# Optimization experiments

Measured on AMD Instinct MI355X. Metric: run time of the kernel, lower is better.

Reference implementation:

```python
import jax, jax.numpy as jnp
import numpy as np

USER_NUM = 100000
ITEM_NUM = 50000
EMBED = 64
N_LAYERS = 3
E_RATE = 2000000
E_TRUST = 500000
E_PRED = 100000


def setup_inputs() -> dict:
    key = jax.random.key(0)
    ks = jax.random.split(key, 10)
    return {
        "emb_user": jax.random.normal(ks[0], (USER_NUM, EMBED), dtype=jnp.float32),
        "emb_item": jax.random.normal(ks[1], (ITEM_NUM, EMBED), dtype=jnp.float32),
        "rate_u": jax.random.randint(ks[2], (E_RATE,), 0, USER_NUM, dtype=jnp.int32),
        "rate_i": jax.random.randint(ks[3], (E_RATE,), 0, ITEM_NUM, dtype=jnp.int32),
        "trust_src": jax.random.randint(ks[4], (E_TRUST,), 0, USER_NUM, dtype=jnp.int32),
        "trust_dst": jax.random.randint(ks[5], (E_TRUST,), 0, USER_NUM, dtype=jnp.int32),
        "pos_u": jax.random.randint(ks[6], (E_PRED,), 0, USER_NUM, dtype=jnp.int32),
        "pos_i": jax.random.randint(ks[7], (E_PRED,), 0, ITEM_NUM, dtype=jnp.int32),
        "neg_u": jax.random.randint(ks[8], (E_PRED,), 0, USER_NUM, dtype=jnp.int32),
        "neg_i": jax.random.randint(ks[9], (E_PRED,), 0, ITEM_NUM, dtype=jnp.int32),
    }


def _degrees(idx, n):
    # float degree counts, clamped to >=1 (DGL GraphConv clamps zero degrees)
    d = jax.ops.segment_sum(jnp.ones_like(idx, dtype=jnp.float32), idx, num_segments=n)
    return jnp.maximum(d, 1.0)


def _gcn_conv(h_src, src, dst, n_dst, deg_src, deg_dst):
    # GraphConv(norm='both', weight=False, bias=False):
    # out[v] = deg(v)^-1/2 * sum_{u->v} deg(u)^-1/2 * h[u]
    ns = jax.lax.rsqrt(deg_src)
    nd = jax.lax.rsqrt(deg_dst)
    msg = (h_src * ns[:, None])[src]          # [E, D] gather
    agg = jax.ops.segment_sum(msg, dst, num_segments=n_dst)
    return agg * nd[:, None]


def reference(emb_user, emb_item, rate_u, rate_i, trust_src, trust_dst,
              pos_u, pos_i, neg_u, neg_i):
    nU, nI = emb_user.shape[0], emb_item.shape[0]
    deg_u = _degrees(rate_u, nU)       # user degree in rate graph (out for rate, in for rated-by)
    deg_i = _degrees(rate_i, nI)       # item degree in rate graph
    deg_ts = _degrees(trust_src, nU)
    deg_td = _degrees(trust_dst, nU)

    res_u, res_i = emb_user, emb_item
    cur_u, cur_i = emb_user, emb_item
    for _ in range(N_LAYERS):
        # item -> user ('rated-by'): src deg = deg_i, dst deg = deg_u
        new_u = _gcn_conv(cur_i, rate_i, rate_u, nU, deg_i, deg_u)
        # user -> item ('rate')
        new_i = _gcn_conv(cur_u, rate_u, rate_i, nI, deg_u, deg_i)
        # user -> user ('trust'), added into user output
        new_u = new_u + _gcn_conv(cur_u, trust_src, trust_dst, nU, deg_ts, deg_td)
        res_u = res_u + new_u
        res_i = res_i + new_i
        cur_u, cur_i = new_u, new_i

    scale = 1.0 / (N_LAYERS + 1)
    res_u = res_u * scale
    res_i = res_i * scale

    # HeteroDotProductPredictor on 'rate' etype: u_dot_v -> [E, 1]
    pos_score = jnp.sum(res_u[pos_u] * res_i[pos_i], axis=-1, keepdims=True)
    neg_score = jnp.sum(res_u[neg_u] * res_i[neg_i], axis=-1, keepdims=True)
    return pos_score, neg_score
```

## Files before the change

kernel.cpp:

```cpp
#include <hip/hip_runtime.h>
#include <hip/hip_fp16.h>

#define NU 100000
#define NI 50000
#define D  64
#define CAPU 64
#define CAPI 96
#define CAPT 32
#define BS 256

#define NB1 256
#define KPB1 391
#define CAPB1 9216
#define NB2 256
#define KPB2 196
#define CAPB2 9216
#define NB3 128
#define KPB3 782
#define CAPB3 4864
#define NB4 128
#define CAPB4 4864
#define GR 224
#define GT 32

typedef unsigned long long u64;

__global__ void __launch_bounds__(1024) k_binAll(
    const int* __restrict__ ru, const int* __restrict__ ri,
    const int* __restrict__ ts, const int* __restrict__ td,
    int* __restrict__ bc1, int* __restrict__ bc2,
    int* __restrict__ bc3, int* __restrict__ bc4,
    u64* __restrict__ bins1, u64* __restrict__ bins2,
    u64* __restrict__ bins3, u64* __restrict__ bins4,
    int E_rate, int E_trust)
{
    __shared__ int cnt[512];
    __shared__ int base[512];
    int b = blockIdx.x, tid = threadIdx.x;
    if (b < GR) {
        if (tid < 512) cnt[tid] = 0;
        __syncthreads();
        for (int c0 = b * 1024; c0 < E_rate; c0 += GR * 1024) {
            int e = c0 + tid;
            if (e < E_rate) {
                int u = ru[e], it = ri[e];
                atomicAdd(&cnt[u / KPB1], 1);
                atomicAdd(&cnt[256 + it / KPB2], 1);
            }
        }
        __syncthreads();
        if (tid < 256)      base[tid] = atomicAdd(&bc1[tid], cnt[tid]);
        else if (tid < 512) base[tid] = atomicAdd(&bc2[tid - 256], cnt[tid]);
        __syncthreads();
        if (tid < 512) cnt[tid] = 0;
        __syncthreads();
        for (int c0 = b * 1024; c0 < E_rate; c0 += GR * 1024) {
            int e = c0 + tid;
            if (e < E_rate) {
                int u = ru[e], it = ri[e];
                int b1 = u / KPB1, b2 = it / KPB2;
                int r1 = atomicAdd(&cnt[b1], 1);
                int o1 = base[b1] + r1;
                if (o1 < CAPB1) bins1[(size_t)b1 * CAPB1 + o1] = ((u64)u << 32) | (unsigned)it;
                int r2 = atomicAdd(&cnt[256 + b2], 1);
                int o2 = base[256 + b2] + r2;
                if (o2 < CAPB2) bins2[(size_t)b2 * CAPB2 + o2] = ((u64)it << 32) | (unsigned)u;
            }
        }
    } else {
        int bb = b - GR;
        if (tid < 256) cnt[tid] = 0;
        __syncthreads();
        for (int c0 = bb * 1024; c0 < E_trust; c0 += GT * 1024) {
            int e = c0 + tid;
            if (e < E_trust) {
                int s = ts[e], dd = td[e];
                atomicAdd(&cnt[dd / KPB3], 1);
                atomicAdd(&cnt[128 + s / KPB3], 1);
            }
        }
        __syncthreads();
        if (tid < 128)      base[tid] = atomicAdd(&bc3[tid], cnt[tid]);
        else if (tid < 256) base[tid] = atomicAdd(&bc4[tid - 128], cnt[tid]);
        __syncthreads();
        if (tid < 256) cnt[tid] = 0;
        __syncthreads();
        for (int c0 = bb * 1024; c0 < E_trust; c0 += GT * 1024) {
            int e = c0 + tid;
            if (e < E_trust) {
                int s = ts[e], dd = td[e];
                int b3 = dd / KPB3, b4 = s / KPB3;
                int r3 = atomicAdd(&cnt[b3], 1);
                int o3 = base[b3] + r3;
                if (o3 < CAPB3) bins3[(size_t)b3 * CAPB3 + o3] = ((u64)dd << 32) | (unsigned)s;
                int r4 = atomicAdd(&cnt[128 + b4], 1);
                int o4 = base[128 + b4] + r4;
                if (o4 < CAPB4) bins4[(size_t)b4 * CAPB4 + o4] = ((u64)s << 32);
            }
        }
    }
}

__global__ void __launch_bounds__(512) k_buildAll(
    const u64* __restrict__ bins1, const u64* __restrict__ bins2,
    const u64* __restrict__ bins3, const u64* __restrict__ bins4,
    const int* __restrict__ bc1, const int* __restrict__ bc2,
    const int* __restrict__ bc3, const int* __restrict__ bc4,
    int* __restrict__ colU, int* __restrict__ colI, int* __restrict__ colT,
    int* __restrict__ degU, int* __restrict__ degI,
    int* __restrict__ degT, int* __restrict__ degS)
{
    __shared__ int cnt[KPB3];
    int b = blockIdx.x, tid = threadIdx.x;
    const u64* bins; int n, k0, kpb, colcap, nmax; int* col; int* deg;
    if (b < NB1) {
        bins = bins1 + (size_t)b * CAPB1; n = bc1[b]; if (n > CAPB1) n = CAPB1;
        k0 = b * KPB1; kpb = KPB1; colcap = CAPU; col = colU; deg = degU; nmax = NU;
    } else if (b < NB1 + NB2) {
        int q = b - NB1;
        bins = bins2 + (size_t)q * CAPB2; n = bc2[q]; if (n > CAPB2) n = CAPB2;
        k0 = q * KPB2; kpb = KPB2; colcap = CAPI; col = colI; deg = degI; nmax = NI;
    } else if (b < NB1 + NB2 + NB3) {
        int q = b - NB1 - NB2;
        bins = bins3 + (size_t)q * CAPB3; n = bc3[q]; if (n > CAPB3) n = CAPB3;
        k0 = q * KPB3; kpb = KPB3; colcap = CAPT; col = colT; deg = degT; nmax = NU;
    } else {
        int q = b - NB1 - NB2 - NB3;
        bins = bins4 + (size_t)q * CAPB4; n = bc4[q]; if (n > CAPB4) n = CAPB4;
        k0 = q * KPB3; kpb = KPB3; colcap = 0; col = nullptr; deg = degS; nmax = NU;
    }
    for (int t = tid; t < kpb; t += 512) cnt[t] = 0;
    __syncthreads();
    if (col) {
        for (int i = tid; i < n; i += 512) {
            u64 e = bins[i];
            int k = (int)(e >> 32);
            int v = (int)(e & 0xffffffffu);
            int c = atomicAdd(&cnt[k - k0], 1);
            if (c < colcap) col[(size_t)k * colcap + c] = v;
        }
    } else {
        for (int i = tid; i < n; i += 512) {
            int k = (int)(bins[i] >> 32);
            atomicAdd(&cnt[k - k0], 1);
        }
    }
    __syncthreads();
    for (int t = tid; t < kpb; t += 512) {
        int k = k0 + t;
        if (k < nmax) {
            int c = cnt[t];
            if (colcap && c > colcap) c = colcap;
            deg[k] = c;
        }
    }
}

__global__ void k_degrs(const int* __restrict__ degU, const int* __restrict__ degI,
                        const int* __restrict__ degT, const int* __restrict__ degS,
                        float* __restrict__ rs_u, float* __restrict__ rs_i,
                        float* __restrict__ rs_td, float* __restrict__ rs_tsu) {
    int i = blockIdx.x * blockDim.x + threadIdx.x;
    if (i < NU) {
        int a = degU[i]; float ru = rsqrtf((float)(a < 1 ? 1 : a));
        rs_u[i] = ru;
        int b = degT[i]; rs_td[i] = rsqrtf((float)(b < 1 ? 1 : b));
        int c = degS[i]; rs_tsu[i] = rsqrtf((float)(c < 1 ? 1 : c)) / ru;
    }
    if (i < NI) {
        int a = degI[i]; rs_i[i] = rsqrtf((float)(a < 1 ? 1 : a));
    }
}

__device__ __forceinline__ uint2 pack4(float a, float b, float c, float d) {
    __half2 lo = __floats2half2_rn(a, b);
    __half2 hi = __floats2half2_rn(c, d);
    uint2 r;
    r.x = *(unsigned*)&lo;
    r.y = *(unsigned*)&hi;
    return r;
}

__global__ void k_inith(const float* __restrict__ src, const float* __restrict__ rs,
                        uint2* __restrict__ curS, uint2* __restrict__ res, int n16) {
    int i = blockIdx.x * blockDim.x + threadIdx.x;
    if (i >= n16) return;
    float4 v = ((const float4*)src)[i];
    float s = rs[i >> 4];
    res[i]  = pack4(v.x, v.y, v.z, v.w);
    curS[i] = pack4(s * v.x, s * v.y, s * v.z, s * v.w);
}

__global__ void k_zrow(uint2* uA, uint2* uB, uint2* iA, uint2* iB) {
    int t = threadIdx.x;
    int e = t & 15;
    uint2 z; z.x = 0; z.y = 0;
    if (t < 16)      uA[(size_t)NU * 16 + e] = z;
    else if (t < 32) uB[(size_t)NU * 16 + e] = z;
    else if (t < 48) iA[(size_t)NI * 16 + e] = z;
    else             iB[(size_t)NI * 16 + e] = z;
}

__global__ void k_layer(const int* __restrict__ colU, const int* __restrict__ degU,
                        const int* __restrict__ colT, const int* __restrict__ degT,
                        const int* __restrict__ colI, const int* __restrict__ degI,
                        const float* __restrict__ rs_u, const float* __restrict__ rs_i,
                        const float* __restrict__ rs_td, const float* __restrict__ rs_tsu,
                        const uint2* __restrict__ cuR, const uint2* __restrict__ ciS,
                        uint2* __restrict__ nuR, uint2* __restrict__ niS,
                        uint2* __restrict__ resu, uint2* __restrict__ resi) {
    int b = blockIdx.x;
    int m = b % 3;
    int base = b / 3;
    int wid = threadIdx.x >> 6;
    int lane = threadIdx.x & 63;
    int grp = lane >> 4;
    int gl  = lane & 15;
    if (m < 2) {
        int node = ((base * 2 + m) * 4 + wid) * 4 + grp;
        if (node >= NU) return;
        float4 acc = {0.f, 0.f, 0.f, 0.f};
        {
            int bb = node * CAPU, e = bb + degU[node];
            for (int k0 = bb; k0 < e; k0 += 16) {
                int idx = k0 + gl;
                int n = idx < e ? colU[idx] : NI;
                #pragma unroll
                for (int j = 0; j < 16; ++j) {
                    int nn = __shfl(n, j, 16);
                    uint2 q = ciS[(size_t)nn * 16 + gl];
                    float2 f = __half22float2(*(__half2*)&q.x);
                    float2 g = __half22float2(*(__half2*)&q.y);
                    acc.x += f.x; acc.y += f.y; acc.z += g.x; acc.w += g.y;
                }
            }
        }
        float4 acc2 = {0.f, 0.f, 0.f, 0.f};
        {
            int bb = node * CAPT, e = bb + degT[node];
            int sub = gl & 7;
            for (int k0 = bb; k0 < e; k0 += 8) {
                int idx = k0 + sub;
                int n = idx < e ? colT[idx] : NU;
                float w = idx < e ? rs_tsu[n] : 0.f;
                #pragma unroll
                for (int j = 0; j < 8; ++j) {
                    int nn  = __shfl(n, j, 16);
                    float ww = __shfl(w, j, 16);
                    uint2 q = cuR[(size_t)nn * 16 + gl];
                    float2 f = __half22float2(*(__half2*)&q.x);
                    float2 g = __half22float2(*(__half2*)&q.y);
                    acc2.x += ww * f.x; acc2.y += ww * f.y;
                    acc2.z += ww * g.x; acc2.w += ww * g.y;
                }
            }
        }
        float su = rs_u[node], st = rs_td[node];
        float vx = su * acc.x + st * acc2.x;
        float vy = su * acc.y + st * acc2.y;
        float vz = su * acc.z + st * acc2.z;
        float vw = su * acc.w + st * acc2.w;
        size_t o = (size_t)node * 16 + gl;
        nuR[o] = pack4(su * vx, su * vy, su * vz, su * vw);
        uint2 r = resu[o];
        float2 ra = __half22float2(*(__half2*)&r.x);
        float2 rb = __half22float2(*(__half2*)&r.y);
        resu[o] = pack4(ra.x + vx, ra.y + vy, rb.x + vz, rb.y + vw);
    } else {
        int node = (base * 4 + wid) * 4 + grp;
        if (node >= NI) return;
        float4 acc = {0.f, 0.f, 0.f, 0.f};
        {
            int bb = node * CAPI, e = bb + degI[node];
            for (int k0 = bb; k0 < e; k0 += 16) {
                int idx = k0 + gl;
                int n = idx < e ? colI[idx] : NU;
                #pragma unroll
                for (int j = 0; j < 16; ++j) {
                    int nn = __shfl(n, j, 16);
                    uint2 q = cuR[(size_t)nn * 16 + gl];
                    float2 f = __half22float2(*(__half2*)&q.x);
                    float2 g = __half22float2(*(__half2*)&q.y);
                    acc.x += f.x; acc.y += f.y; acc.z += g.x; acc.w += g.y;
                }
            }
        }
        float si = rs_i[node];
        float vx = si * acc.x, vy = si * acc.y, vz = si * acc.z, vw = si * acc.w;
        size_t o = (size_t)node * 16 + gl;
        niS[o] = pack4(si * vx, si * vy, si * vz, si * vw);
        uint2 r = resi[o];
        float2 ra = __half22float2(*(__half2*)&r.x);
        float2 rb = __half22float2(*(__half2*)&r.y);
        resi[o] = pack4(ra.x + vx, ra.y + vy, rb.x + vz, rb.y + vw);
    }
}

__global__ void k_pred(const int* __restrict__ pu, const int* __restrict__ pi,
                       const int* __restrict__ nuv, const int* __restrict__ niv,
                       const __half2* __restrict__ ru, const __half2* __restrict__ ri,
                       float* __restrict__ out, int E) {
    long long tid = (long long)blockIdx.x * blockDim.x + threadIdx.x;
    int e = (int)(tid >> 4);
    int c2 = ((int)tid & 15) * 2;
    if (e >= 2 * E) return;
    int ee = (e < E) ? e : e - E;
    int u  = (e < E) ? pu[ee] : nuv[ee];
    int it = (e < E) ? pi[ee] : niv[ee];
    float2 a0 = __half22float2(ru[(size_t)u  * 32 + c2]);
    float2 a1 = __half22float2(ru[(size_t)u  * 32 + c2 + 1]);
    float2 b0 = __half22float2(ri[(size_t)it * 32 + c2]);
    float2 b1 = __half22float2(ri[(size_t)it * 32 + c2 + 1]);
    float s = a0.x * b0.x + a0.y * b0.y + a1.x * b1.x + a1.y * b1.y;
    s += __shfl_xor(s, 1); s += __shfl_xor(s, 2);
    s += __shfl_xor(s, 4); s += __shfl_xor(s, 8);
    if (((int)tid & 15) == 0) out[e] = s * (1.0f / 16.0f);
}

extern "C" void kernel_launch(void* const* d_in, const int* in_sizes, int n_in,
                              void* d_out, int out_size, void* d_ws, size_t ws_size,
                              hipStream_t stream) {
    const float* emb_u  = (const float*)d_in[0];
    const float* emb_i  = (const float*)d_in[1];
    const int* rate_u   = (const int*)d_in[2];
    const int* rate_i   = (const int*)d_in[3];
    const int* trust_s  = (const int*)d_in[4];
    const int* trust_d  = (const int*)d_in[5];
    const int* pos_u    = (const int*)d_in[6];
    const int* pos_i    = (const int*)d_in[7];
    const int* neg_u    = (const int*)d_in[8];
    const int* neg_i    = (const int*)d_in[9];
    const int E_rate  = in_sizes[2];
    const int E_trust = in_sizes[4];
    const int E_pred  = in_sizes[6];

    int* iw   = (int*)d_ws;
    int* degU = iw;
    int* degI = degU + NU;
    int* degT = degI + NI;
    int* degS = degT + NU;
    int* bc1  = degS + NU;
    int* bc2  = bc1 + NB1;
    int* bc3  = bc2 + NB2;
    int* bc4  = bc3 + NB3;
    int* colU = bc4 + NB4;
    int* colI = colU + (size_t)NU * CAPU;
    int* colT = colI + (size_t)NI * CAPI;
    float* rs_u   = (float*)(colT + (size_t)NU * CAPT);
    float* rs_i   = rs_u  + NU;
    float* rs_td  = rs_i  + NI;
    float* rs_tsu = rs_td + NU;
    uint2* uRA  = (uint2*)(rs_tsu + NU);
    uint2* uRB  = uRA + (size_t)(NU + 1) * 16;
    uint2* iSA  = uRB + (size_t)(NU + 1) * 16;
    uint2* iSB  = iSA + (size_t)(NI + 1) * 16;
    uint2* res_u = iSB + (size_t)(NI + 1) * 16;
    uint2* res_i = res_u + (size_t)NU * 16;
    u64* bins1 = (u64*)uRA;
    u64* bins2 = bins1 + (size_t)NB1 * CAPB1;
    u64* bins3 = bins2 + (size_t)NB2 * CAPB2;
    u64* bins4 = bins3 + (size_t)NB3 * CAPB3;

    hipMemsetAsync(bc1, 0, (NB1 + NB2 + NB3 + NB4) * sizeof(int), stream);

    k_binAll<<<GR + GT, 1024, 0, stream>>>(rate_u, rate_i, trust_s, trust_d,
                                           bc1, bc2, bc3, bc4,
                                           bins1, bins2, bins3, bins4,
                                           E_rate, E_trust);
    k_buildAll<<<NB1 + NB2 + NB3 + NB4, 512, 0, stream>>>(
        bins1, bins2, bins3, bins4, bc1, bc2, bc3, bc4,
        colU, colI, colT, degU, degI, degT, degS);

    k_degrs<<<(NU + BS - 1) / BS, BS, 0, stream>>>(degU, degI, degT, degS,
                                                   rs_u, rs_i, rs_td, rs_tsu);

    k_inith<<<(NU * 16 + BS - 1) / BS, BS, 0, stream>>>(emb_u, rs_u, uRA, res_u, NU * 16);
    k_inith<<<(NI * 16 + BS - 1) / BS, BS, 0, stream>>>(emb_i, rs_i, iSA, res_i, NI * 16);
    k_zrow<<<1, 64, 0, stream>>>(uRA, uRB, iSA, iSB);

    uint2* cu = uRA; uint2* nu_ = uRB;
    uint2* ci = iSA; uint2* ni_ = iSB;
    for (int l = 0; l < 3; ++l) {
        k_layer<<<9375, BS, 0, stream>>>(colU, degU, colT, degT, colI, degI,
                                         rs_u, rs_i, rs_td, rs_tsu,
                                         cu, ci, nu_, ni_, res_u, res_i);
        uint2* t;
        t = cu; cu = nu_; nu_ = t;
        t = ci; ci = ni_; ni_ = t;
    }

    long long tp = (long long)2 * E_pred * 16;
    k_pred<<<(unsigned)((tp + BS - 1) / BS), BS, 0, stream>>>(
        pos_u, pos_i, neg_u, neg_i, (const __half2*)res_u, (const __half2*)res_i,
        (float*)d_out, E_pred);
}
```

Baseline: 366.3 us.

## Pack bins into 32-bit keys, shrink user adjacency to u16, accumulate in half2

Bin entries are packed into 32-bit words holding a local key offset plus the neighbour index, halving bin traffic. The user adjacency list of item ids is stored as 16-bit values, halving those index loads. The layer kernel accumulates rating-neighbour sums in half2 instead of float, and the binning grid is enlarged fourfold. The half-precision accumulation over up to 64-96 neighbours risks precision loss and overflow.

```diff
diff --git a/kernel.cpp b/kernel.cpp
--- a/kernel.cpp
+++ b/kernel.cpp
@@ -3,7 +3,6 @@
 
 #define NU 100000
 #define NI 50000
-#define D  64
 #define CAPU 64
 #define CAPI 96
 #define CAPT 32
@@ -20,18 +19,19 @@
 #define CAPB3 4864
 #define NB4 128
 #define CAPB4 4864
-#define GR 224
-#define GT 32
-
-typedef unsigned long long u64;
+#define GR 896
+#define GT 128
+
+typedef unsigned int u32;
+typedef unsigned short u16;
 
 __global__ void __launch_bounds__(1024) k_binAll(
     const int* __restrict__ ru, const int* __restrict__ ri,
     const int* __restrict__ ts, const int* __restrict__ td,
     int* __restrict__ bc1, int* __restrict__ bc2,
     int* __restrict__ bc3, int* __restrict__ bc4,
-    u64* __restrict__ bins1, u64* __restrict__ bins2,
-    u64* __restrict__ bins3, u64* __restrict__ bins4,
+    u32* __restrict__ bins1, u32* __restrict__ bins2,
+    u32* __restrict__ bins3, u32* __restrict__ bins4,
     int E_rate, int E_trust)
 {
     __shared__ int cnt[512];
@@ -61,10 +61,12 @@
                 int b1 = u / KPB1, b2 = it / KPB2;
                 int r1 = atomicAdd(&cnt[b1], 1);
                 int o1 = base[b1] + r1;
-                if (o1 < CAPB1) bins1[(size_t)b1 * CAPB1 + o1] = ((u64)u << 32) | (unsigned)it;
+                if (o1 < CAPB1)
+                    bins1[(size_t)b1 * CAPB1 + o1] = ((u32)(u - b1 * KPB1) << 16) | (u32)it;
                 int r2 = atomicAdd(&cnt[256 + b2], 1);
                 int o2 = base[256 + b2] + r2;
-                if (o2 < CAPB2) bins2[(size_t)b2 * CAPB2 + o2] = ((u64)it << 32) | (unsigned)u;
+                if (o2 < CAPB2)
+                    bins2[(size_t)b2 * CAPB2 + o2] = ((u32)(it - b2 * KPB2) << 17) | (u32)u;
             }
         }
     } else {
@@ -92,66 +94,93 @@
                 int b3 = dd / KPB3, b4 = s / KPB3;
                 int r3 = atomicAdd(&cnt[b3], 1);
                 int o3 = base[b3] + r3;
-                if (o3 < CAPB3) bins3[(size_t)b3 * CAPB3 + o3] = ((u64)dd << 32) | (unsigned)s;
+                if (o3 < CAPB3)
+                    bins3[(size_t)b3 * CAPB3 + o3] = ((u32)(dd - b3 * KPB3) << 17) | (u32)s;
                 int r4 = atomicAdd(&cnt[128 + b4], 1);
                 int o4 = base[128 + b4] + r4;
-                if (o4 < CAPB4) bins4[(size_t)b4 * CAPB4 + o4] = ((u64)s << 32);
+                if (o4 < CAPB4)
+                    bins4[(size_t)b4 * CAPB4 + o4] = (u32)(s - b4 * KPB3);
             }
         }
     }
 }
 
 __global__ void __launch_bounds__(512) k_buildAll(
-    const u64* __restrict__ bins1, const u64* __restrict__ bins2,
-    const u64* __restrict__ bins3, const u64* __restrict__ bins4,
+    const u32* __restrict__ bins1, const u32* __restrict__ bins2,
+    const u32* __restrict__ bins3, const u32* __restrict__ bins4,
     const int* __restrict__ bc1, const int* __restrict__ bc2,
     const int* __restrict__ bc3, const int* __restrict__ bc4,
-    int* __restrict__ colU, int* __restrict__ colI, int* __restrict__ colT,
+    u16* __restrict__ colU, int* __restrict__ colI, int* __restrict__ colT,
     int* __restrict__ degU, int* __restrict__ degI,
     int* __restrict__ degT, int* __restrict__ degS)
 {
     __shared__ int cnt[KPB3];
     int b = blockIdx.x, tid = threadIdx.x;
-    const u64* bins; int n, k0, kpb, colcap, nmax; int* col; int* deg;
     if (b < NB1) {
-        bins = bins1 + (size_t)b * CAPB1; n = bc1[b]; if (n > CAPB1) n = CAPB1;
-        k0 = b * KPB1; kpb = KPB1; colcap = CAPU; col = colU; deg = degU; nmax = NU;
+        const u32* bins = bins1 + (size_t)b * CAPB1;
+        int n = bc1[b]; if (n > CAPB1) n = CAPB1;
+        int k0 = b * KPB1;
+        for (int t = tid; t < KPB1; t += 512) cnt[t] = 0;
+        __syncthreads();
+        for (int i = tid; i < n; i += 512) {
+            u32 e = bins[i];
+            int ko = e >> 16, v = e & 0xFFFF;
+            int c = atomicAdd(&cnt[ko], 1);
+            if (c < CAPU) colU[(size_t)(k0 + ko) * CAPU + c] = (u16)v;
+        }
+        __syncthreads();
+        for (int t = tid; t < KPB1; t += 512) {
+            int k = k0 + t;
+            if (k < NU) { int c = cnt[t]; if (c > CAPU) c = CAPU; degU[k] = c; }
+        }
     } else if (b < NB1 + NB2) {
         int q = b - NB1;
-        bins = bins2 + (size_t)q * CAPB2; n = bc2[q]; if (n > CAPB2) n = CAPB2;
-        k0 = q * KPB2; kpb = KPB2; colcap = CAPI; col = colI; deg = degI; nmax = NI;
+        const u32* bins = bins2 + (size_t)q * CAPB2;
+        int n = bc2[q]; if (n > CAPB2) n = CAPB2;
+        int k0 = q * KPB2;
+        for (int t = tid; t < KPB2; t += 512) cnt[t] = 0;
+        __syncthreads();
+        for (int i = tid; i < n; i += 512) {
+            u32 e = bins[i];
+            int ko = e >> 17, v = e & 0x1FFFF;
+            int c = atomicAdd(&cnt[ko], 1);
+            if (c < CAPI) colI[(size_t)(k0 + ko) * CAPI + c] = v;
+        }
+        __syncthreads();
+        for (int t = tid; t < KPB2; t += 512) {
+            int k = k0 + t;
+            if (k < NI) { int c = cnt[t]; if (c > CAPI) c = CAPI; degI[k] = c; }
+        }
     } else if (b < NB1 + NB2 + NB3) {
         int q = b - NB1 - NB2;
-        bins = bins3 + (size_t)q * CAPB3; n = bc3[q]; if (n > CAPB3) n = CAPB3;
-        k0 = q * KPB3; kpb = KPB3; colcap = CAPT; col = colT; deg = degT; nmax = NU;
+        const u32* bins = bins3 + (size_t)q * CAPB3;
+        int n = bc3[q]; if (n > CAPB3) n = CAPB3;
+        int k0 = q * KPB3;
+        for (int t = tid; t < KPB3; t += 512) cnt[t] = 0;
+        __syncthreads();
+        for (int i = tid; i < n; i += 512) {
+            u32 e = bins[i];
+            int ko = e >> 17, v = e & 0x1FFFF;
+            int c = atomicAdd(&cnt[ko], 1);
+            if (c < CAPT) colT[(size_t)(k0 + ko) * CAPT + c] = v;
+        }
+        __syncthreads();
+        for (int t = tid; t < KPB3; t += 512) {
+            int k = k0 + t;
+            if (k < NU) { int c = cnt[t]; if (c > CAPT) c = CAPT; degT[k] = c; }
+        }
     } else {
         int q = b - NB1 - NB2 - NB3;
-        bins = bins4 + (size_t)q * CAPB4; n = bc4[q]; if (n > CAPB4) n = CAPB4;
-        k0 = q * KPB3; kpb = KPB3; colcap = 0; col = nullptr; deg = degS; nmax = NU;
-    }
-    for (int t = tid; t < kpb; t += 512) cnt[t] = 0;
-    __syncthreads();
-    if (col) {
-        for (int i = tid; i < n; i += 512) {
-            u64 e = bins[i];
-            int k = (int)(e >> 32);
-            int v = (int)(e & 0xffffffffu);
-            int c = atomicAdd(&cnt[k - k0], 1);
-            if (c < colcap) col[(size_t)k * colcap + c] = v;
-        }
-    } else {
-        for (int i = tid; i < n; i += 512) {
-            int k = (int)(bins[i] >> 32);
-            atomicAdd(&cnt[k - k0], 1);
-        }
-    }
-    __syncthreads();
-    for (int t = tid; t < kpb; t += 512) {
-        int k = k0 + t;
-        if (k < nmax) {
-            int c = cnt[t];
-            if (colcap && c > colcap) c = colcap;
-            deg[k] = c;
+        const u32* bins = bins4 + (size_t)q * CAPB4;
+        int n = bc4[q]; if (n > CAPB4) n = CAPB4;
+        int k0 = q * KPB3;
+        for (int t = tid; t < KPB3; t += 512) cnt[t] = 0;
+        __syncthreads();
+        for (int i = tid; i < n; i += 512) atomicAdd(&cnt[bins[i]], 1);
+        __syncthreads();
+        for (int t = tid; t < KPB3; t += 512) {
+            int k = k0 + t;
+            if (k < NU) degS[k] = cnt[t];
         }
     }
 }
@@ -201,7 +230,7 @@
     else             iB[(size_t)NI * 16 + e] = z;
 }
 
-__global__ void k_layer(const int* __restrict__ colU, const int* __restrict__ degU,
+__global__ void k_layer(const u16* __restrict__ colU, const int* __restrict__ degU,
                         const int* __restrict__ colT, const int* __restrict__ degT,
                         const int* __restrict__ colI, const int* __restrict__ degI,
                         const float* __restrict__ rs_u, const float* __restrict__ rs_i,
@@ -216,25 +245,26 @@
     int lane = threadIdx.x & 63;
     int grp = lane >> 4;
     int gl  = lane & 15;
+    __half2 zero = __floats2half2_rn(0.f, 0.f);
     if (m < 2) {
         int node = ((base * 2 + m) * 4 + wid) * 4 + grp;
         if (node >= NU) return;
-        float4 acc = {0.f, 0.f, 0.f, 0.f};
+        __half2 ha = zero, hb = zero;
         {
             int bb = node * CAPU, e = bb + degU[node];
             for (int k0 = bb; k0 < e; k0 += 16) {
                 int idx = k0 + gl;
-                int n = idx < e ? colU[idx] : NI;
+                int n = idx < e ? (int)colU[idx] : NI;
                 #pragma unroll
                 for (int j = 0; j < 16; ++j) {
                     int nn = __shfl(n, j, 16);
                     uint2 q = ciS[(size_t)nn * 16 + gl];
-                    float2 f = __half22float2(*(__half2*)&q.x);
-                    float2 g = __half22float2(*(__half2*)&q.y);
-                    acc.x += f.x; acc.y += f.y; acc.z += g.x; acc.w += g.y;
+                    ha = __hadd2(ha, *(__half2*)&q.x);
+                    hb = __hadd2(hb, *(__half2*)&q.y);
                 }
             }
         }
+        float2 fa = __half22float2(ha), fb = __half22float2(hb);
         float4 acc2 = {0.f, 0.f, 0.f, 0.f};
         {
             int bb = node * CAPT, e = bb + degT[node];
@@ -256,10 +286,10 @@
             }
         }
         float su = rs_u[node], st = rs_td[node];
-        float vx = su * acc.x + st * acc2.x;
-        float vy = su * acc.y + st * acc2.y;
-        float vz = su * acc.z + st * acc2.z;
-        float vw = su * acc.w + st * acc2.w;
+        float vx = su * fa.x + st * acc2.x;
+        float vy = su * fa.y + st * acc2.y;
+        float vz = su * fb.x + st * acc2.z;
+        float vw = su * fb.y + st * acc2.w;
         size_t o = (size_t)node * 16 + gl;
         nuR[o] = pack4(su * vx, su * vy, su * vz, su * vw);
         uint2 r = resu[o];
@@ -269,7 +299,7 @@
     } else {
         int node = (base * 4 + wid) * 4 + grp;
         if (node >= NI) return;
-        float4 acc = {0.f, 0.f, 0.f, 0.f};
+        __half2 ha = zero, hb = zero;
         {
             int bb = node * CAPI, e = bb + degI[node];
             for (int k0 = bb; k0 < e; k0 += 16) {
@@ -279,14 +309,14 @@
                 for (int j = 0; j < 16; ++j) {
                     int nn = __shfl(n, j, 16);
                     uint2 q = cuR[(size_t)nn * 16 + gl];
-                    float2 f = __half22float2(*(__half2*)&q.x);
-                    float2 g = __half22float2(*(__half2*)&q.y);
-                    acc.x += f.x; acc.y += f.y; acc.z += g.x; acc.w += g.y;
+                    ha = __hadd2(ha, *(__half2*)&q.x);
+                    hb = __hadd2(hb, *(__half2*)&q.y);
                 }
             }
         }
+        float2 fa = __half22float2(ha), fb = __half22float2(hb);
         float si = rs_i[node];
-        float vx = si * acc.x, vy = si * acc.y, vz = si * acc.z, vw = si * acc.w;
+        float vx = si * fa.x, vy = si * fa.y, vz = si * fb.x, vw = si * fb.y;
         size_t o = (size_t)node * 16 + gl;
         niS[o] = pack4(si * vx, si * vy, si * vz, si * vw);
         uint2 r = resi[o];
@@ -343,8 +373,8 @@
     int* bc2  = bc1 + NB1;
     int* bc3  = bc2 + NB2;
     int* bc4  = bc3 + NB3;
-    int* colU = bc4 + NB4;
-    int* colI = colU + (size_t)NU * CAPU;
+    u16* colU = (u16*)(bc4 + NB4);
+    int* colI = (int*)(colU + (size_t)NU * CAPU);
     int* colT = colI + (size_t)NI * CAPI;
     float* rs_u   = (float*)(colT + (size_t)NU * CAPT);
     float* rs_i   = rs_u  + NU;
@@ -356,10 +386,10 @@
     uint2* iSB  = iSA + (size_t)(NI + 1) * 16;
     uint2* res_u = iSB + (size_t)(NI + 1) * 16;
     uint2* res_i = res_u + (size_t)NU * 16;
-    u64* bins1 = (u64*)uRA;
-    u64* bins2 = bins1 + (size_t)NB1 * CAPB1;
-    u64* bins3 = bins2 + (size_t)NB2 * CAPB2;
-    u64* bins4 = bins3 + (size_t)NB3 * CAPB3;
+    u32* bins1 = (u32*)uRA;
+    u32* bins2 = bins1 + (size_t)NB1 * CAPB1;
+    u32* bins3 = bins2 + (size_t)NB2 * CAPB2;
+    u32* bins4 = bins3 + (size_t)NB3 * CAPB3;
 
     hipMemsetAsync(bc1, 0, (NB1 + NB2 + NB3 + NB4) * sizeof(int), stream);
 
```

Measured after the change: 354.5 us. -3.2%, faster.
